# Kernel optimization log

Measured on AMD Instinct MI355X. Metric: run time of the kernel, lower is better.

## Reference

```python
import jax, jax.numpy as jnp
import numpy as np

# Shapes / hyperparams (match init_kwargs and input_specs)
B, CIN, COUT, H, W = 8, 128, 128, 64, 64
K, S, P, D = 3, 1, 1, 1
KK = K * K
EPS = 1e-5  # BatchNorm eps


def setup_inputs() -> dict:
    key = jax.random.key(0)
    ks = jax.random.split(key, 4)
    x = jax.random.normal(ks[0], (B, CIN, H, W), jnp.float32)
    # small offset weights so predicted offsets stay O(1) pixels
    w_off = jax.random.normal(ks[1], (2 * KK, CIN, K, K), jnp.float32) * 0.01
    w_def = jax.random.normal(ks[2], (COUT, CIN, K, K), jnp.float32) * (1.0 / np.sqrt(CIN * KK))
    b_def = jax.random.normal(ks[3], (COUT,), jnp.float32) * 0.01
    gamma = jnp.ones((COUT,), jnp.float32)
    beta = jnp.zeros((COUT,), jnp.float32)
    return dict(x=x, w_off=w_off, w_def=w_def, b_def=b_def, gamma=gamma, beta=beta)


def _bilinear_gather(x, ys, xs):
    """x: [B,C,H,W]; ys/xs: [B,KK,Ho,Wo] float coords -> [B,C,KK,Ho,Wo].
    Zero padding outside the image (torchvision DeformConv2d semantics)."""
    Bb, C, Hh, Ww = x.shape
    y0 = jnp.floor(ys)
    x0 = jnp.floor(xs)
    wy = ys - y0
    wx = xs - x0
    xf = x.reshape(Bb, C, Hh * Ww)

    def gather(yi, xi, w):
        valid = (yi >= 0) & (yi < Hh) & (xi >= 0) & (xi < Ww)
        idx = (jnp.clip(yi, 0, Hh - 1) * Ww + jnp.clip(xi, 0, Ww - 1)).astype(jnp.int32)
        g = jnp.take_along_axis(xf, idx.reshape(Bb, 1, -1), axis=2)  # [B,C,KK*Ho*Wo]
        g = g.reshape(Bb, C, *idx.shape[1:])  # [B,C,KK,Ho,Wo]
        return g * (w * valid)[:, None]

    return (gather(y0, x0, (1 - wy) * (1 - wx))
            + gather(y0, x0 + 1, (1 - wy) * wx)
            + gather(y0 + 1, x0, wy * (1 - wx))
            + gather(y0 + 1, x0 + 1, wy * wx))


def _forward(x, w_off, w_def, b_def, gamma, beta):
    # 1) offset prediction: standard conv, no bias
    offset = jax.lax.conv_general_dilated(
        x, w_off, window_strides=(S, S), padding=((P, P), (P, P)),
        rhs_dilation=(D, D), dimension_numbers=('NCHW', 'OIHW', 'NCHW'))
    Ho, Wo = offset.shape[2], offset.shape[3]
    off = offset.reshape(B, KK, 2, Ho, Wo)  # (dy, dx) pairs per kernel loc
    dy, dx = off[:, :, 0], off[:, :, 1]

    # 2) deformable sampling coordinates
    ky = (jnp.arange(KK) // K).astype(jnp.float32) * D  # kernel row offset
    kx = (jnp.arange(KK) % K).astype(jnp.float32) * D   # kernel col offset
    base_y = (jnp.arange(Ho) * S - P).astype(jnp.float32)
    base_x = (jnp.arange(Wo) * S - P).astype(jnp.float32)
    ys = base_y[None, None, :, None] + ky[None, :, None, None] + dy  # [B,KK,Ho,Wo]
    xs = base_x[None, None, None, :] + kx[None, :, None, None] + dx

    sampled = _bilinear_gather(x, ys, xs)  # [B,CIN,KK,Ho,Wo]

    # 3) per-kernel-location weighted accumulation (implicit GEMM) + bias
    out = jnp.einsum('bckhw,ock->bohw', sampled, w_def.reshape(COUT, CIN, KK))
    out = out + b_def[None, :, None, None]

    # 4) BatchNorm2d (training mode: batch statistics) + SiLU
    mean = out.mean(axis=(0, 2, 3))
    var = out.var(axis=(0, 2, 3))
    scale = gamma / jnp.sqrt(var + EPS)
    out = (out - mean[None, :, None, None]) * scale[None, :, None, None] + beta[None, :, None, None]
    return out * jax.nn.sigmoid(out)  # SiLU


def reference(x, w_off, w_def, b_def, gamma, beta):
    return _forward(x, w_off, w_def, b_def, gamma, beta)
```

## Files before the change

kernel.cpp:

```cpp
#include <hip/hip_runtime.h>
#include <math.h>

#define CIN   128
#define COUT  128
#define KKT   9
#define NSTAT 32768.0f

typedef __attribute__((ext_vector_type(8))) short bf16x8;
typedef __attribute__((ext_vector_type(4))) float f32x4;

__device__ inline unsigned short f2bf(float f) {
    union { float f; unsigned u; } v; v.f = f;
    unsigned r = v.u + 0x7fffu + ((v.u >> 16) & 1u);
    return (unsigned short)(r >> 16);
}
__device__ inline float bflo(unsigned u) { union { unsigned u; float f; } v; v.u = u << 16; return v.f; }
__device__ inline float bfhi(unsigned u) { union { unsigned u; float f; } v; v.u = u & 0xffff0000u; return v.f; }

#define FAST_BARRIER() asm volatile("s_waitcnt lgkmcnt(0)\n\ts_barrier" ::: "memory")


__global__ __launch_bounds__(512) void prep_xt_k(const float* __restrict__ x,
                                                 unsigned* __restrict__ xt) {
    __shared__ float lt[128][65];
    const int by = blockIdx.x;
    const int b = by >> 6, y = by & 63;
    const int t = threadIdx.x, l = t & 63, g8 = t >> 6;
    const float* xb = x + (b * 128) * 4096 + y * 64;
#pragma unroll
    for (int pass = 0; pass < 16; pass++) {
        int c = pass * 8 + g8;
        lt[c][l] = xb[c * 4096 + l];
    }
    __syncthreads();
    unsigned* xo = xt + (by * 64) * 64;
#pragma unroll
    for (int pass = 0; pass < 8; pass++) {
        int w = pass * 8 + g8;
        float f0 = lt[2 * l][w], f1 = lt[2 * l + 1][w];
        xo[w * 64 + l] = (unsigned)f2bf(f0) | ((unsigned)f2bf(f1) << 16);
    }
}

__global__ __launch_bounds__(256) void repack_w_k(const float* __restrict__ w_def,
                                                  const float* __restrict__ w_off,
                                                  unsigned short* __restrict__ wb,
                                                  unsigned short* __restrict__ wob,
                                                  float* __restrict__ sums) {
    int i = blockIdx.x * 256 + threadIdx.x;
    if (i < 147456) {
        int oc = i / 1152, r = i - oc * 1152, kt = r >> 7, c = r & 127;
        wb[i] = f2bf(w_def[(oc * 128 + c) * 9 + kt]);
    } else if (i < 147456 + 36864) {
        int j = i - 147456;
        int ocp = j / 1152, r = j - ocp * 1152, kt = r >> 7, c = r & 127;
        wob[j] = (ocp < 18) ? f2bf(w_off[(ocp * 128 + c) * 9 + kt]) : (unsigned short)0;
    } else if (i < 147456 + 36864 + 256) {
        sums[i - 147456 - 36864] = 0.f;
    }
}

#define RB 51200
__global__ __launch_bounds__(512, 4) void deform_main_k(const unsigned* __restrict__ xt,
                                                        const unsigned short* __restrict__ wb,
                                                        const unsigned short* __restrict__ wob,
                                                        const float* __restrict__ b_def,
                                                        float* __restrict__ out,
                                                        float* __restrict__ sums,
                                                        float* __restrict__ sumsq) {
    __shared__ __align__(16) unsigned char smem[RB + 4608 + 1024];
    unsigned short* xrow = (unsigned short*)smem;
    int*            tab  = (int*)smem;
    unsigned short* samp0 = (unsigned short*)(smem + 18432);
    unsigned short* samp1 = (unsigned short*)(smem + 34816);
    float* offl = (float*)(smem + RB);
    float* stat = (float*)(smem + RB + 4608);

    const int t    = threadIdx.x;
    const int bh   = blockIdx.x;
    const int b    = bh >> 6;
    const int j_   = bh & 63;
    const int h    = ((j_ & 7) << 3) | (j_ >> 3);
    const int lane = t & 63;
    const int wv   = __builtin_amdgcn_readfirstlane(t >> 6);
    const int quad = lane >> 4, lo = lane & 15;
    const int l    = lane;
    const int g    = lane >> 2;

    if (t < 256) stat[t] = 0.f;

    const unsigned* xtb = xt + b * 262144;

    for (int p = wv; p < 198; p += 8) {
        int r = p / 66, xi = p - r * 66;
        int y = h + r - 1, x = xi - 1;
        unsigned u = 0;
        if ((unsigned)y < 64u && (unsigned)x < 64u) u = xtb[(y * 64 + x) * 64 + l];
        ((unsigned*)xrow)[(r * 66 + xi) * 64 + ((g ^ (xi & 15)) << 2) + (l & 3)] = u;
    }
    __syncthreads();

    {
        const int mt = wv >> 2, nt = wv & 3;
        f32x4 ao = {0.f, 0.f, 0.f, 0.f};
        const unsigned short* wrow = wob + (mt * 16 + lo) * 1152 + quad * 8;
        for (int kt = 0; kt < 9; kt++) {
            int ky = kt / 3, kx = kt - ky * 3;
            int xi = nt * 16 + lo + kx;
#pragma unroll
            for (int ch = 0; ch < 4; ch++) {
                int gg = ch * 4 + quad;
                bf16x8 af = *(const bf16x8*)(wrow + kt * 128 + ch * 32);
                bf16x8 bf = *(const bf16x8*)(xrow + (ky * 66 + xi) * 128 + ((gg ^ (xi & 15)) << 3));
                ao = __builtin_amdgcn_mfma_f32_16x16x32_bf16(af, bf, ao, 0, 0, 0);
            }
        }
        __syncthreads();
#pragma unroll
        for (int r = 0; r < 4; r++) {
            int oc = mt * 16 + quad * 4 + r;
            if (oc < 18) offl[oc * 64 + nt * 16 + lo] = ao[r];
        }
    }
    __syncthreads();

    for (int i = t; i < KKT * 64; i += 512) {
        int k = i >> 6, w2 = i & 63;
        float dy = offl[(2 * k) * 64 + w2];
        float dx = offl[(2 * k + 1) * 64 + w2];
        int ky = k / 3, kx = k - ky * 3;
        float ys = (float)(h - 1 + ky) + dy;
        float xs = (float)(w2 - 1 + kx) + dx;
        float y0f = floorf(ys), x0f = floorf(xs);
        float wyf = ys - y0f, wxf = xs - x0f;
        int iy0 = (int)y0f, ix0 = (int)x0f;
        int cy0 = min(max(iy0, 0), 63), cy1 = min(max(iy0 + 1, 0), 63);
        int px  = min(max(ix0, 0), 63), px2 = min(max(ix0 + 1, 0), 63);
        float wy0 = (iy0 >= 0 && iy0 < 64) ? (1.f - wyf) : 0.f;
        float wy1 = (iy0 + 1 >= 0 && iy0 + 1 < 64) ? wyf : 0.f;
        float wa  = (ix0 >= 0 && ix0 < 64) ? (1.f - wxf) : 0.f;
        float wbv = (ix0 + 1 >= 0 && ix0 + 1 < 64) ? wxf : 0.f;
        int base = i * 8;
        tab[base + 0] = (cy0 * 64 + px ) * 64;
        tab[base + 1] = (cy0 * 64 + px2) * 64;
        tab[base + 2] = (cy1 * 64 + px ) * 64;
        tab[base + 3] = (cy1 * 64 + px2) * 64;
        ((float*)tab)[base + 4] = wy0;
        ((float*)tab)[base + 5] = wy1;
        ((float*)tab)[base + 6] = wa;
        ((float*)tab)[base + 7] = wbv;
    }
    __syncthreads();

    const int m0 = wv >> 1, n0 = wv & 1;
    f32x4 acc[2][2];
#pragma unroll
    for (int i = 0; i < 2; i++)
#pragma unroll
        for (int j = 0; j < 2; j++)
#pragma unroll
            for (int r = 0; r < 4; r++) acc[i][j][r] = 0.f;

    const unsigned short* wrow0 = wb + (2 * m0 * 16 + lo) * 1152 + quad * 8;
    const unsigned short* wrow1 = wrow0 + 16 * 1152;

    for (int kt = 0; kt < KKT; kt++) {
        bf16x8 af0[4], af1[4];
#pragma unroll
        for (int ch = 0; ch < 4; ch++) {
            af0[ch] = *(const bf16x8*)(wrow0 + kt * 128 + ch * 32);
            af1[ch] = *(const bf16x8*)(wrow1 + kt * 128 + ch * 32);
        }
        unsigned* sb = (unsigned*)((kt & 1) ? samp1 : samp0);
#pragma unroll
        for (int i = 0; i < 8; i++) {
            int w = wv * 8 + i;
            int bse = (kt * 64 + w) * 8;
            int4   ta = *(const int4*)&tab[bse];
            float4 tw = *(const float4*)&tab[bse + 4];
            unsigned u00 = xtb[ta.x + l];
            unsigned u01 = xtb[ta.y + l];
            unsigned u10 = xtb[ta.z + l];
            unsigned u11 = xtb[ta.w + l];
            float e = tw.x * (tw.z * bflo(u00) + tw.w * bflo(u01)) +
                      tw.y * (tw.z * bflo(u10) + tw.w * bflo(u11));
            float o = tw.x * (tw.z * bfhi(u00) + tw.w * bfhi(u01)) +
                      tw.y * (tw.z * bfhi(u10) + tw.w * bfhi(u11));
            sb[w * 64 + ((g ^ (w & 15)) << 2) + (l & 3)] =
                (unsigned)f2bf(e) | ((unsigned)f2bf(o) << 16);
        }
        FAST_BARRIER();
        const unsigned short* sbs = (kt & 1) ? samp1 : samp0;
#pragma unroll
        for (int ch = 0; ch < 4; ch++) {
            int gg = ch * 4 + quad;
            int r0 = (2 * n0 + 0) * 16 + lo, r1 = (2 * n0 + 1) * 16 + lo;
            bf16x8 bf0 = *(const bf16x8*)(sbs + r0 * 128 + ((gg ^ lo) << 3));
            bf16x8 bf1 = *(const bf16x8*)(sbs + r1 * 128 + ((gg ^ lo) << 3));
            acc[0][0] = __builtin_amdgcn_mfma_f32_16x16x32_bf16(af0[ch], bf0, acc[0][0], 0, 0, 0);
            acc[0][1] = __builtin_amdgcn_mfma_f32_16x16x32_bf16(af0[ch], bf1, acc[0][1], 0, 0, 0);
            acc[1][0] = __builtin_amdgcn_mfma_f32_16x16x32_bf16(af1[ch], bf0, acc[1][0], 0, 0, 0);
            acc[1][1] = __builtin_amdgcn_mfma_f32_16x16x32_bf16(af1[ch], bf1, acc[1][1], 0, 0, 0);
        }
    }

    float* ob = out + b * COUT * 4096 + h * 64;
#pragma unroll
    for (int mt2 = 0; mt2 < 2; mt2++) {
        int ocb = (2 * m0 + mt2) * 16 + quad * 4;
#pragma unroll
        for (int r = 0; r < 4; r++) {
            int oc = ocb + r;
            float bia = b_def[oc];
            float ssum = 0.f, qsum = 0.f;
#pragma unroll
            for (int nt2 = 0; nt2 < 2; nt2++) {
                int w_ = (2 * n0 + nt2) * 16 + lo;
                float v = acc[mt2][nt2][r] + bia;
                ob[oc * 4096 + w_] = v;
                ssum += v; qsum += v * v;
            }
#pragma unroll
            for (int d = 1; d < 16; d <<= 1) {
                ssum += __shfl_xor(ssum, d, 64);
                qsum += __shfl_xor(qsum, d, 64);
            }
            if (lo == 0) { atomicAdd(&stat[oc], ssum); atomicAdd(&stat[128 + oc], qsum); }
        }
    }
    __syncthreads();
    if (t < 256) {
        float* gp = (t < 128) ? (sums + t) : (sumsq + (t - 128));
        atomicAdd(gp, stat[t]);
    }
}

__global__ __launch_bounds__(256) void bn_silu_k(float* __restrict__ out,
                                                 const float* __restrict__ sums,
                                                 const float* __restrict__ sumsq,
                                                 const float* __restrict__ gamma,
                                                 const float* __restrict__ beta) {
    __shared__ float sc_s[128], sh_s[128];
    int t = threadIdx.x;
    if (t < 128) {
        const float invN = 1.f / NSTAT;
        float m = sums[t] * invN;
        float v = fmaf(-m, m, sumsq[t] * invN);
        float sc = gamma[t] * rsqrtf(v + 1e-5f);
        sc_s[t] = sc;
        sh_s[t] = beta[t] - m * sc;
    }
    __syncthreads();
    int i = blockIdx.x * 256 + t;
    float4 v = ((float4*)out)[i];
    int oc = (i >> 10) & 127;
    float sc = sc_s[oc], sh = sh_s[oc];
    float z0 = v.x * sc + sh;
    float z1 = v.y * sc + sh;
    float z2 = v.z * sc + sh;
    float z3 = v.w * sc + sh;
    v.x = z0 / (1.f + __expf(-z0));
    v.y = z1 / (1.f + __expf(-z1));
    v.z = z2 / (1.f + __expf(-z2));
    v.w = z3 / (1.f + __expf(-z3));
    ((float4*)out)[i] = v;
}

extern "C" void kernel_launch(void* const* d_in, const int* in_sizes, int n_in,
                              void* d_out, int out_size, void* d_ws, size_t ws_size,
                              hipStream_t stream) {
    const float* x     = (const float*)d_in[0];
    const float* w_off = (const float*)d_in[1];
    const float* w_def = (const float*)d_in[2];
    const float* b_def = (const float*)d_in[3];
    const float* gamma = (const float*)d_in[4];
    const float* beta  = (const float*)d_in[5];
    float* out = (float*)d_out;

    unsigned*       xt   = (unsigned*)d_ws;
    unsigned short* wb   = (unsigned short*)((char*)d_ws + 16777216);
    unsigned short* wob  = (unsigned short*)((char*)d_ws + 17072128);
    float*          sums = (float*)((char*)d_ws + 17145856);
    float*          sumsq = sums + 128;

    prep_xt_k<<<512, 512, 0, stream>>>(x, xt);
    repack_w_k<<<721, 256, 0, stream>>>(w_def, w_off, wb, wob, sums);
    deform_main_k<<<512, 512, 0, stream>>>(xt, wb, wob, b_def, out, sums, sumsq);
    bn_silu_k<<<4096, 256, 0, stream>>>(out, sums, sumsq, gamma, beta);
}
```

Measured before the change: 167.9 us.

## Merge prep kernels and software-pipeline gather and weight loads across kernel taps

The input transpose and the weight repack kernels become a single launch, removing one kernel launch and its gap. In the main deformable conv loop, the four bilinear-corner gathers and the weight fragments for the next tap are issued before the barrier and MFMA phase of the current tap, so their memory latency overlaps with compute. This holds 32 extra gathered words plus the weight fragments in registers, which may reduce occupancy under the 512x4 launch bound or cause spills.

```diff
diff --git a/kernel.cpp b/kernel.cpp
--- a/kernel.cpp
+++ b/kernel.cpp
@@ -20,43 +20,45 @@
 #define FAST_BARRIER() asm volatile("s_waitcnt lgkmcnt(0)\n\ts_barrier" ::: "memory")
 
 
-__global__ __launch_bounds__(512) void prep_xt_k(const float* __restrict__ x,
-                                                 unsigned* __restrict__ xt) {
-    __shared__ float lt[128][65];
-    const int by = blockIdx.x;
-    const int b = by >> 6, y = by & 63;
-    const int t = threadIdx.x, l = t & 63, g8 = t >> 6;
-    const float* xb = x + (b * 128) * 4096 + y * 64;
-#pragma unroll
-    for (int pass = 0; pass < 16; pass++) {
-        int c = pass * 8 + g8;
-        lt[c][l] = xb[c * 4096 + l];
-    }
-    __syncthreads();
-    unsigned* xo = xt + (by * 64) * 64;
-#pragma unroll
-    for (int pass = 0; pass < 8; pass++) {
-        int w = pass * 8 + g8;
-        float f0 = lt[2 * l][w], f1 = lt[2 * l + 1][w];
-        xo[w * 64 + l] = (unsigned)f2bf(f0) | ((unsigned)f2bf(f1) << 16);
-    }
-}
-
-__global__ __launch_bounds__(256) void repack_w_k(const float* __restrict__ w_def,
+__global__ __launch_bounds__(512) void prep_all_k(const float* __restrict__ x,
+                                                  const float* __restrict__ w_def,
                                                   const float* __restrict__ w_off,
+                                                  unsigned* __restrict__ xt,
                                                   unsigned short* __restrict__ wb,
                                                   unsigned short* __restrict__ wob,
                                                   float* __restrict__ sums) {
-    int i = blockIdx.x * 256 + threadIdx.x;
-    if (i < 147456) {
-        int oc = i / 1152, r = i - oc * 1152, kt = r >> 7, c = r & 127;
-        wb[i] = f2bf(w_def[(oc * 128 + c) * 9 + kt]);
-    } else if (i < 147456 + 36864) {
-        int j = i - 147456;
-        int ocp = j / 1152, r = j - ocp * 1152, kt = r >> 7, c = r & 127;
-        wob[j] = (ocp < 18) ? f2bf(w_off[(ocp * 128 + c) * 9 + kt]) : (unsigned short)0;
-    } else if (i < 147456 + 36864 + 256) {
-        sums[i - 147456 - 36864] = 0.f;
+    const int blk = blockIdx.x;
+    if (blk < 512) {
+        __shared__ float lt[128][65];
+        const int by = blk;
+        const int b = by >> 6, y = by & 63;
+        const int t = threadIdx.x, l = t & 63, g8 = t >> 6;
+        const float* xb = x + (b * 128) * 4096 + y * 64;
+#pragma unroll
+        for (int pass = 0; pass < 16; pass++) {
+            int c = pass * 8 + g8;
+            lt[c][l] = xb[c * 4096 + l];
+        }
+        __syncthreads();
+        unsigned* xo = xt + (by * 64) * 64;
+#pragma unroll
+        for (int pass = 0; pass < 8; pass++) {
+            int w = pass * 8 + g8;
+            float f0 = lt[2 * l][w], f1 = lt[2 * l + 1][w];
+            xo[w * 64 + l] = (unsigned)f2bf(f0) | ((unsigned)f2bf(f1) << 16);
+        }
+    } else {
+        int i = (blk - 512) * 512 + threadIdx.x;
+        if (i < 147456) {
+            int oc = i / 1152, r = i - oc * 1152, kt = r >> 7, c = r & 127;
+            wb[i] = f2bf(w_def[(oc * 128 + c) * 9 + kt]);
+        } else if (i < 147456 + 36864) {
+            int j = i - 147456;
+            int ocp = j / 1152, r = j - ocp * 1152, kt = r >> 7, c = r & 127;
+            wob[j] = (ocp < 18) ? f2bf(w_off[(ocp * 128 + c) * 9 + kt]) : (unsigned short)0;
+        } else if (i < 147456 + 36864 + 256) {
+            sums[i - 147456 - 36864] = 0.f;
+        }
     }
 }
 
@@ -164,24 +166,32 @@
     const unsigned short* wrow0 = wb + (2 * m0 * 16 + lo) * 1152 + quad * 8;
     const unsigned short* wrow1 = wrow0 + 16 * 1152;
 
+    unsigned gr[32];
+    bf16x8 afA[4], afB[4];
+
+#pragma unroll
+    for (int i = 0; i < 8; i++) {
+        int w = wv * 8 + i;
+        int4 ta = *(const int4*)&tab[(0 * 64 + w) * 8];
+        gr[i * 4 + 0] = xtb[ta.x + l];
+        gr[i * 4 + 1] = xtb[ta.y + l];
+        gr[i * 4 + 2] = xtb[ta.z + l];
+        gr[i * 4 + 3] = xtb[ta.w + l];
+    }
+#pragma unroll
+    for (int ch = 0; ch < 4; ch++) {
+        afA[ch] = *(const bf16x8*)(wrow0 + 0 * 128 + ch * 32);
+        afB[ch] = *(const bf16x8*)(wrow1 + 0 * 128 + ch * 32);
+    }
+
     for (int kt = 0; kt < KKT; kt++) {
-        bf16x8 af0[4], af1[4];
-#pragma unroll
-        for (int ch = 0; ch < 4; ch++) {
-            af0[ch] = *(const bf16x8*)(wrow0 + kt * 128 + ch * 32);
-            af1[ch] = *(const bf16x8*)(wrow1 + kt * 128 + ch * 32);
-        }
         unsigned* sb = (unsigned*)((kt & 1) ? samp1 : samp0);
 #pragma unroll
         for (int i = 0; i < 8; i++) {
             int w = wv * 8 + i;
-            int bse = (kt * 64 + w) * 8;
-            int4   ta = *(const int4*)&tab[bse];
-            float4 tw = *(const float4*)&tab[bse + 4];
-            unsigned u00 = xtb[ta.x + l];
-            unsigned u01 = xtb[ta.y + l];
-            unsigned u10 = xtb[ta.z + l];
-            unsigned u11 = xtb[ta.w + l];
+            float4 tw = *(const float4*)&tab[(kt * 64 + w) * 8 + 4];
+            unsigned u00 = gr[i * 4 + 0], u01 = gr[i * 4 + 1];
+            unsigned u10 = gr[i * 4 + 2], u11 = gr[i * 4 + 3];
             float e = tw.x * (tw.z * bflo(u00) + tw.w * bflo(u01)) +
                       tw.y * (tw.z * bflo(u10) + tw.w * bflo(u11));
             float o = tw.x * (tw.z * bfhi(u00) + tw.w * bfhi(u01)) +
@@ -189,6 +199,17 @@
             sb[w * 64 + ((g ^ (w & 15)) << 2) + (l & 3)] =
                 (unsigned)f2bf(e) | ((unsigned)f2bf(o) << 16);
         }
+        if (kt < KKT - 1) {
+#pragma unroll
+            for (int i = 0; i < 8; i++) {
+                int w = wv * 8 + i;
+                int4 ta = *(const int4*)&tab[((kt + 1) * 64 + w) * 8];
+                gr[i * 4 + 0] = xtb[ta.x + l];
+                gr[i * 4 + 1] = xtb[ta.y + l];
+                gr[i * 4 + 2] = xtb[ta.z + l];
+                gr[i * 4 + 3] = xtb[ta.w + l];
+            }
+        }
         FAST_BARRIER();
         const unsigned short* sbs = (kt & 1) ? samp1 : samp0;
 #pragma unroll
@@ -197,10 +218,17 @@
             int r0 = (2 * n0 + 0) * 16 + lo, r1 = (2 * n0 + 1) * 16 + lo;
             bf16x8 bf0 = *(const bf16x8*)(sbs + r0 * 128 + ((gg ^ lo) << 3));
             bf16x8 bf1 = *(const bf16x8*)(sbs + r1 * 128 + ((gg ^ lo) << 3));
-            acc[0][0] = __builtin_amdgcn_mfma_f32_16x16x32_bf16(af0[ch], bf0, acc[0][0], 0, 0, 0);
-            acc[0][1] = __builtin_amdgcn_mfma_f32_16x16x32_bf16(af0[ch], bf1, acc[0][1], 0, 0, 0);
-            acc[1][0] = __builtin_amdgcn_mfma_f32_16x16x32_bf16(af1[ch], bf0, acc[1][0], 0, 0, 0);
-            acc[1][1] = __builtin_amdgcn_mfma_f32_16x16x32_bf16(af1[ch], bf1, acc[1][1], 0, 0, 0);
+            acc[0][0] = __builtin_amdgcn_mfma_f32_16x16x32_bf16(afA[ch], bf0, acc[0][0], 0, 0, 0);
+            acc[0][1] = __builtin_amdgcn_mfma_f32_16x16x32_bf16(afA[ch], bf1, acc[0][1], 0, 0, 0);
+            acc[1][0] = __builtin_amdgcn_mfma_f32_16x16x32_bf16(afB[ch], bf0, acc[1][0], 0, 0, 0);
+            acc[1][1] = __builtin_amdgcn_mfma_f32_16x16x32_bf16(afB[ch], bf1, acc[1][1], 0, 0, 0);
+        }
+        if (kt < KKT - 1) {
+#pragma unroll
+            for (int ch = 0; ch < 4; ch++) {
+                afA[ch] = *(const bf16x8*)(wrow0 + (kt + 1) * 128 + ch * 32);
+                afB[ch] = *(const bf16x8*)(wrow1 + (kt + 1) * 128 + ch * 32);
+            }
         }
     }
 
@@ -283,8 +311,7 @@
     float*          sums = (float*)((char*)d_ws + 17145856);
     float*          sumsq = sums + 128;
 
-    prep_xt_k<<<512, 512, 0, stream>>>(x, xt);
-    repack_w_k<<<721, 256, 0, stream>>>(w_def, w_off, wb, wob, sums);
+    prep_all_k<<<873, 512, 0, stream>>>(x, w_def, w_off, xt, wb, wob, sums);
     deform_main_k<<<512, 512, 0, stream>>>(xt, wb, wob, b_def, out, sums, sumsq);
     bn_silu_k<<<4096, 256, 0, stream>>>(out, sums, sumsq, gamma, beta);
 }
```

After: 181.7 us. +8.2%, slower.

## Gather deformable samples directly into MFMA registers, drop LDS staging and merge prep kernels

Applied to the files above, without the earlier changes.

The main kernel now uses 256 threads. Each wave owns 16 output columns and all 128 output channels. The offset conv and the bilinear sampling read x straight from global memory into MFMA B-fragments in registers, instead of staging the input rows and sampled tiles in LDS behind per-tap barriers. The two prep kernels are merged into one launch, and bf16 packing uses a cheaper rounding. In exchange there are more redundant global/L2 loads, many more weight fragment loads per wave, more register pressure from 8 accumulators, and slightly different bf16 rounding.

```diff
diff --git a/kernel.cpp b/kernel.cpp
--- a/kernel.cpp
+++ b/kernel.cpp
@@ -9,6 +9,8 @@
 typedef __attribute__((ext_vector_type(8))) short bf16x8;
 typedef __attribute__((ext_vector_type(4))) float f32x4;
 
+union U4B { uint4 u; bf16x8 b; };
+
 __device__ inline unsigned short f2bf(float f) {
     union { float f; unsigned u; } v; v.f = f;
     unsigned r = v.u + 0x7fffu + ((v.u >> 16) & 1u);
@@ -16,65 +18,65 @@
 }
 __device__ inline float bflo(unsigned u) { union { unsigned u; float f; } v; v.u = u << 16; return v.f; }
 __device__ inline float bfhi(unsigned u) { union { unsigned u; float f; } v; v.u = u & 0xffff0000u; return v.f; }
-
-#define FAST_BARRIER() asm volatile("s_waitcnt lgkmcnt(0)\n\ts_barrier" ::: "memory")
-
-
-__global__ __launch_bounds__(512) void prep_xt_k(const float* __restrict__ x,
-                                                 unsigned* __restrict__ xt) {
-    __shared__ float lt[128][65];
-    const int by = blockIdx.x;
-    const int b = by >> 6, y = by & 63;
-    const int t = threadIdx.x, l = t & 63, g8 = t >> 6;
-    const float* xb = x + (b * 128) * 4096 + y * 64;
-#pragma unroll
-    for (int pass = 0; pass < 16; pass++) {
-        int c = pass * 8 + g8;
-        lt[c][l] = xb[c * 4096 + l];
-    }
-    __syncthreads();
-    unsigned* xo = xt + (by * 64) * 64;
-#pragma unroll
-    for (int pass = 0; pass < 8; pass++) {
-        int w = pass * 8 + g8;
-        float f0 = lt[2 * l][w], f1 = lt[2 * l + 1][w];
-        xo[w * 64 + l] = (unsigned)f2bf(f0) | ((unsigned)f2bf(f1) << 16);
-    }
-}
-
-__global__ __launch_bounds__(256) void repack_w_k(const float* __restrict__ w_def,
+__device__ inline unsigned pk2bf(float e, float o) {
+    union { float f; unsigned u; } a, b; a.f = e; b.f = o;
+    return ((a.u + 0x8000u) >> 16) | ((b.u + 0x8000u) & 0xffff0000u);
+}
+
+
+__global__ __launch_bounds__(512) void prep_all_k(const float* __restrict__ x,
+                                                  const float* __restrict__ w_def,
                                                   const float* __restrict__ w_off,
+                                                  unsigned* __restrict__ xt,
                                                   unsigned short* __restrict__ wb,
                                                   unsigned short* __restrict__ wob,
                                                   float* __restrict__ sums) {
-    int i = blockIdx.x * 256 + threadIdx.x;
-    if (i < 147456) {
-        int oc = i / 1152, r = i - oc * 1152, kt = r >> 7, c = r & 127;
-        wb[i] = f2bf(w_def[(oc * 128 + c) * 9 + kt]);
-    } else if (i < 147456 + 36864) {
-        int j = i - 147456;
-        int ocp = j / 1152, r = j - ocp * 1152, kt = r >> 7, c = r & 127;
-        wob[j] = (ocp < 18) ? f2bf(w_off[(ocp * 128 + c) * 9 + kt]) : (unsigned short)0;
-    } else if (i < 147456 + 36864 + 256) {
-        sums[i - 147456 - 36864] = 0.f;
-    }
-}
-
-#define RB 51200
-__global__ __launch_bounds__(512, 4) void deform_main_k(const unsigned* __restrict__ xt,
+    const int blk = blockIdx.x;
+    if (blk < 512) {
+        __shared__ float lt[128][65];
+        const int by = blk;
+        const int b = by >> 6, y = by & 63;
+        const int t = threadIdx.x, l = t & 63, g8 = t >> 6;
+        const float* xb = x + (b * 128) * 4096 + y * 64;
+#pragma unroll
+        for (int pass = 0; pass < 16; pass++) {
+            int c = pass * 8 + g8;
+            lt[c][l] = xb[c * 4096 + l];
+        }
+        __syncthreads();
+        unsigned* xo = xt + (by * 64) * 64;
+#pragma unroll
+        for (int pass = 0; pass < 8; pass++) {
+            int w = pass * 8 + g8;
+            float f0 = lt[2 * l][w], f1 = lt[2 * l + 1][w];
+            xo[w * 64 + l] = (unsigned)f2bf(f0) | ((unsigned)f2bf(f1) << 16);
+        }
+    } else {
+        int i = (blk - 512) * 512 + threadIdx.x;
+        if (i < 147456) {
+            int oc = i / 1152, r = i - oc * 1152, kt = r >> 7, c = r & 127;
+            wb[i] = f2bf(w_def[(oc * 128 + c) * 9 + kt]);
+        } else if (i < 147456 + 36864) {
+            int j = i - 147456;
+            int ocp = j / 1152, r = j - ocp * 1152, kt = r >> 7, c = r & 127;
+            wob[j] = (ocp < 18) ? f2bf(w_off[(ocp * 128 + c) * 9 + kt]) : (unsigned short)0;
+        } else if (i < 147456 + 36864 + 256) {
+            sums[i - 147456 - 36864] = 0.f;
+        }
+    }
+}
+
+__global__ __launch_bounds__(256, 2) void deform_main_k(const unsigned* __restrict__ xt,
                                                         const unsigned short* __restrict__ wb,
                                                         const unsigned short* __restrict__ wob,
                                                         const float* __restrict__ b_def,
                                                         float* __restrict__ out,
                                                         float* __restrict__ sums,
                                                         float* __restrict__ sumsq) {
-    __shared__ __align__(16) unsigned char smem[RB + 4608 + 1024];
-    unsigned short* xrow = (unsigned short*)smem;
-    int*            tab  = (int*)smem;
-    unsigned short* samp0 = (unsigned short*)(smem + 18432);
-    unsigned short* samp1 = (unsigned short*)(smem + 34816);
-    float* offl = (float*)(smem + RB);
-    float* stat = (float*)(smem + RB + 4608);
+    __shared__ int   taddr[KKT][64][4];
+    __shared__ float twts[KKT][64][4];
+    __shared__ float offl[18][64];
+    __shared__ float stat[256];
 
     const int t    = threadIdx.x;
     const int bh   = blockIdx.x;
@@ -84,50 +86,47 @@
     const int lane = t & 63;
     const int wv   = __builtin_amdgcn_readfirstlane(t >> 6);
     const int quad = lane >> 4, lo = lane & 15;
-    const int l    = lane;
-    const int g    = lane >> 2;
-
-    if (t < 256) stat[t] = 0.f;
+    const int w    = wv * 16 + lo;
+
+    stat[t] = 0.f;
 
     const unsigned* xtb = xt + b * 262144;
 
-    for (int p = wv; p < 198; p += 8) {
-        int r = p / 66, xi = p - r * 66;
-        int y = h + r - 1, x = xi - 1;
-        unsigned u = 0;
-        if ((unsigned)y < 64u && (unsigned)x < 64u) u = xtb[(y * 64 + x) * 64 + l];
-        ((unsigned*)xrow)[(r * 66 + xi) * 64 + ((g ^ (xi & 15)) << 2) + (l & 3)] = u;
-    }
-    __syncthreads();
-
     {
-        const int mt = wv >> 2, nt = wv & 3;
-        f32x4 ao = {0.f, 0.f, 0.f, 0.f};
-        const unsigned short* wrow = wob + (mt * 16 + lo) * 1152 + quad * 8;
+        f32x4 a0 = {0.f, 0.f, 0.f, 0.f}, a1 = {0.f, 0.f, 0.f, 0.f};
+        const unsigned short* wr0 = wob + lo * 1152 + quad * 8;
+        const unsigned short* wr1 = wob + (16 + lo) * 1152 + quad * 8;
         for (int kt = 0; kt < 9; kt++) {
             int ky = kt / 3, kx = kt - ky * 3;
-            int xi = nt * 16 + lo + kx;
+            int y  = h + ky - 1;
+            int xp = w + kx - 1;
+            bool val = ((unsigned)y < 64u) && ((unsigned)xp < 64u);
+            int py = min(max(y, 0), 63), px = min(max(xp, 0), 63);
+            const unsigned* pb = xtb + (py * 64 + px) * 64;
 #pragma unroll
             for (int ch = 0; ch < 4; ch++) {
-                int gg = ch * 4 + quad;
-                bf16x8 af = *(const bf16x8*)(wrow + kt * 128 + ch * 32);
-                bf16x8 bf = *(const bf16x8*)(xrow + (ky * 66 + xi) * 128 + ((gg ^ (xi & 15)) << 3));
-                ao = __builtin_amdgcn_mfma_f32_16x16x32_bf16(af, bf, ao, 0, 0, 0);
-            }
-        }
-        __syncthreads();
+                U4B bu; bu.u = *(const uint4*)(pb + ch * 16 + quad * 4);
+                if (!val) { bu.u.x = 0; bu.u.y = 0; bu.u.z = 0; bu.u.w = 0; }
+                bf16x8 af0 = *(const bf16x8*)(wr0 + kt * 128 + ch * 32);
+                bf16x8 af1 = *(const bf16x8*)(wr1 + kt * 128 + ch * 32);
+                a0 = __builtin_amdgcn_mfma_f32_16x16x32_bf16(af0, bu.b, a0, 0, 0, 0);
+                a1 = __builtin_amdgcn_mfma_f32_16x16x32_bf16(af1, bu.b, a1, 0, 0, 0);
+            }
+        }
 #pragma unroll
         for (int r = 0; r < 4; r++) {
-            int oc = mt * 16 + quad * 4 + r;
-            if (oc < 18) offl[oc * 64 + nt * 16 + lo] = ao[r];
-        }
-    }
-    __syncthreads();
-
-    for (int i = t; i < KKT * 64; i += 512) {
+            int oc0 = quad * 4 + r;
+            if (oc0 < 18) offl[oc0][w] = a0[r];
+            int oc1 = 16 + quad * 4 + r;
+            if (oc1 < 18) offl[oc1][w] = a1[r];
+        }
+    }
+    __syncthreads();
+
+    for (int i = t; i < KKT * 64; i += 256) {
         int k = i >> 6, w2 = i & 63;
-        float dy = offl[(2 * k) * 64 + w2];
-        float dx = offl[(2 * k + 1) * 64 + w2];
+        float dy = offl[2 * k][w2];
+        float dx = offl[2 * k + 1][w2];
         int ky = k / 3, kx = k - ky * 3;
         float ys = (float)(h - 1 + ky) + dy;
         float xs = (float)(w2 - 1 + kx) + dx;
@@ -140,96 +139,89 @@
         float wy1 = (iy0 + 1 >= 0 && iy0 + 1 < 64) ? wyf : 0.f;
         float wa  = (ix0 >= 0 && ix0 < 64) ? (1.f - wxf) : 0.f;
         float wbv = (ix0 + 1 >= 0 && ix0 + 1 < 64) ? wxf : 0.f;
-        int base = i * 8;
-        tab[base + 0] = (cy0 * 64 + px ) * 64;
-        tab[base + 1] = (cy0 * 64 + px2) * 64;
-        tab[base + 2] = (cy1 * 64 + px ) * 64;
-        tab[base + 3] = (cy1 * 64 + px2) * 64;
-        ((float*)tab)[base + 4] = wy0;
-        ((float*)tab)[base + 5] = wy1;
-        ((float*)tab)[base + 6] = wa;
-        ((float*)tab)[base + 7] = wbv;
-    }
-    __syncthreads();
-
-    const int m0 = wv >> 1, n0 = wv & 1;
-    f32x4 acc[2][2];
-#pragma unroll
-    for (int i = 0; i < 2; i++)
-#pragma unroll
-        for (int j = 0; j < 2; j++)
-#pragma unroll
-            for (int r = 0; r < 4; r++) acc[i][j][r] = 0.f;
-
-    const unsigned short* wrow0 = wb + (2 * m0 * 16 + lo) * 1152 + quad * 8;
-    const unsigned short* wrow1 = wrow0 + 16 * 1152;
+        taddr[k][w2][0] = (cy0 * 64 + px ) * 64;
+        taddr[k][w2][1] = (cy0 * 64 + px2) * 64;
+        taddr[k][w2][2] = (cy1 * 64 + px ) * 64;
+        taddr[k][w2][3] = (cy1 * 64 + px2) * 64;
+        twts[k][w2][0] = wy0;
+        twts[k][w2][1] = wy1;
+        twts[k][w2][2] = wa;
+        twts[k][w2][3] = wbv;
+    }
+    __syncthreads();
+
+    f32x4 acc[8];
+#pragma unroll
+    for (int i = 0; i < 8; i++) acc[i] = (f32x4){0.f, 0.f, 0.f, 0.f};
+
+    const unsigned short* wlq = wb + lo * 1152 + quad * 8;
 
     for (int kt = 0; kt < KKT; kt++) {
-        bf16x8 af0[4], af1[4];
+        int4   ta = *(const int4*)&taddr[kt][w][0];
+        float4 tw = *(const float4*)&twts[kt][w][0];
+        float c00 = tw.x * tw.z, c01 = tw.x * tw.w;
+        float c10 = tw.y * tw.z, c11 = tw.y * tw.w;
+        const unsigned* p00 = xtb + ta.x;
+        const unsigned* p01 = xtb + ta.y;
+        const unsigned* p10 = xtb + ta.z;
+        const unsigned* p11 = xtb + ta.w;
+        const unsigned short* wk = wlq + kt * 128;
 #pragma unroll
         for (int ch = 0; ch < 4; ch++) {
-            af0[ch] = *(const bf16x8*)(wrow0 + kt * 128 + ch * 32);
-            af1[ch] = *(const bf16x8*)(wrow1 + kt * 128 + ch * 32);
-        }
-        unsigned* sb = (unsigned*)((kt & 1) ? samp1 : samp0);
-#pragma unroll
-        for (int i = 0; i < 8; i++) {
-            int w = wv * 8 + i;
-            int bse = (kt * 64 + w) * 8;
-            int4   ta = *(const int4*)&tab[bse];
-            float4 tw = *(const float4*)&tab[bse + 4];
-            unsigned u00 = xtb[ta.x + l];
-            unsigned u01 = xtb[ta.y + l];
-            unsigned u10 = xtb[ta.z + l];
-            unsigned u11 = xtb[ta.w + l];
-            float e = tw.x * (tw.z * bflo(u00) + tw.w * bflo(u01)) +
-                      tw.y * (tw.z * bflo(u10) + tw.w * bflo(u11));
-            float o = tw.x * (tw.z * bfhi(u00) + tw.w * bfhi(u01)) +
-                      tw.y * (tw.z * bfhi(u10) + tw.w * bfhi(u11));
-            sb[w * 64 + ((g ^ (w & 15)) << 2) + (l & 3)] =
-                (unsigned)f2bf(e) | ((unsigned)f2bf(o) << 16);
-        }
-        FAST_BARRIER();
-        const unsigned short* sbs = (kt & 1) ? samp1 : samp0;
-#pragma unroll
-        for (int ch = 0; ch < 4; ch++) {
-            int gg = ch * 4 + quad;
-            int r0 = (2 * n0 + 0) * 16 + lo, r1 = (2 * n0 + 1) * 16 + lo;
-            bf16x8 bf0 = *(const bf16x8*)(sbs + r0 * 128 + ((gg ^ lo) << 3));
-            bf16x8 bf1 = *(const bf16x8*)(sbs + r1 * 128 + ((gg ^ lo) << 3));
-            acc[0][0] = __builtin_amdgcn_mfma_f32_16x16x32_bf16(af0[ch], bf0, acc[0][0], 0, 0, 0);
-            acc[0][1] = __builtin_amdgcn_mfma_f32_16x16x32_bf16(af0[ch], bf1, acc[0][1], 0, 0, 0);
-            acc[1][0] = __builtin_amdgcn_mfma_f32_16x16x32_bf16(af1[ch], bf0, acc[1][0], 0, 0, 0);
-            acc[1][1] = __builtin_amdgcn_mfma_f32_16x16x32_bf16(af1[ch], bf1, acc[1][1], 0, 0, 0);
+            int off = ch * 16 + quad * 4;
+            uint4 u00 = *(const uint4*)(p00 + off);
+            uint4 u01 = *(const uint4*)(p01 + off);
+            uint4 u10 = *(const uint4*)(p10 + off);
+            uint4 u11 = *(const uint4*)(p11 + off);
+            U4B bf;
+            {
+                float e = c00 * bflo(u00.x) + c01 * bflo(u01.x) + c10 * bflo(u10.x) + c11 * bflo(u11.x);
+                float o = c00 * bfhi(u00.x) + c01 * bfhi(u01.x) + c10 * bfhi(u10.x) + c11 * bfhi(u11.x);
+                bf.u.x = pk2bf(e, o);
+            }
+            {
+                float e = c00 * bflo(u00.y) + c01 * bflo(u01.y) + c10 * bflo(u10.y) + c11 * bflo(u11.y);
+                float o = c00 * bfhi(u00.y) + c01 * bfhi(u01.y) + c10 * bfhi(u10.y) + c11 * bfhi(u11.y);
+                bf.u.y = pk2bf(e, o);
+            }
+            {
+                float e = c00 * bflo(u00.z) + c01 * bflo(u01.z) + c10 * bflo(u10.z) + c11 * bflo(u11.z);
+                float o = c00 * bfhi(u00.z) + c01 * bfhi(u01.z) + c10 * bfhi(u10.z) + c11 * bfhi(u11.z);
+                bf.u.z = pk2bf(e, o);
+            }
+            {
+                float e = c00 * bflo(u00.w) + c01 * bflo(u01.w) + c10 * bflo(u10.w) + c11 * bflo(u11.w);
+                float o = c00 * bfhi(u00.w) + c01 * bfhi(u01.w) + c10 * bfhi(u10.w) + c11 * bfhi(u11.w);
+                bf.u.w = pk2bf(e, o);
+            }
+            const unsigned short* wkc = wk + ch * 32;
+#pragma unroll
+            for (int mt = 0; mt < 8; mt++) {
+                bf16x8 af = *(const bf16x8*)(wkc + mt * 16 * 1152);
+                acc[mt] = __builtin_amdgcn_mfma_f32_16x16x32_bf16(af, bf.b, acc[mt], 0, 0, 0);
+            }
         }
     }
 
     float* ob = out + b * COUT * 4096 + h * 64;
 #pragma unroll
-    for (int mt2 = 0; mt2 < 2; mt2++) {
-        int ocb = (2 * m0 + mt2) * 16 + quad * 4;
+    for (int mt = 0; mt < 8; mt++) {
 #pragma unroll
         for (int r = 0; r < 4; r++) {
-            int oc = ocb + r;
-            float bia = b_def[oc];
-            float ssum = 0.f, qsum = 0.f;
-#pragma unroll
-            for (int nt2 = 0; nt2 < 2; nt2++) {
-                int w_ = (2 * n0 + nt2) * 16 + lo;
-                float v = acc[mt2][nt2][r] + bia;
-                ob[oc * 4096 + w_] = v;
-                ssum += v; qsum += v * v;
-            }
+            int oc = mt * 16 + quad * 4 + r;
+            float v = acc[mt][r] + b_def[oc];
+            ob[oc * 4096 + w] = v;
+            float s = v, q = v * v;
 #pragma unroll
             for (int d = 1; d < 16; d <<= 1) {
-                ssum += __shfl_xor(ssum, d, 64);
-                qsum += __shfl_xor(qsum, d, 64);
-            }
-            if (lo == 0) { atomicAdd(&stat[oc], ssum); atomicAdd(&stat[128 + oc], qsum); }
-        }
-    }
-    __syncthreads();
-    if (t < 256) {
+                s += __shfl_xor(s, d, 64);
+                q += __shfl_xor(q, d, 64);
+            }
+            if (lo == 0) { atomicAdd(&stat[oc], s); atomicAdd(&stat[128 + oc], q); }
+        }
+    }
+    __syncthreads();
+    {
         float* gp = (t < 128) ? (sums + t) : (sumsq + (t - 128));
         atomicAdd(gp, stat[t]);
     }
@@ -283,8 +275,7 @@
     float*          sums = (float*)((char*)d_ws + 17145856);
     float*          sumsq = sums + 128;
 
-    prep_xt_k<<<512, 512, 0, stream>>>(x, xt);
-    repack_w_k<<<721, 256, 0, stream>>>(w_def, w_off, wb, wob, sums);
-    deform_main_k<<<512, 512, 0, stream>>>(xt, wb, wob, b_def, out, sums, sumsq);
+    prep_all_k<<<873, 512, 0, stream>>>(x, w_def, w_off, xt, wb, wob, sums);
+    deform_main_k<<<512, 256, 0, stream>>>(xt, wb, wob, b_def, out, sums, sumsq);
     bn_silu_k<<<4096, 256, 0, stream>>>(out, sums, sumsq, gamma, beta);
 }
```

Result: slower. 219.1 us (+30.4%).

## Merge prep kernels and drop halo staging to shrink LDS in deform kernel

Applied to the files above, without the earlier changes.

Fuses the x transpose and weight repack kernels into one launch, saving a kernel launch. In the main kernel the offset-prediction conv now reads its B operand straight from global memory instead of staging a 3-row halo in LDS. That shrinks shared memory from about 57KB to roughly 52KB and raises the launch-bounds occupancy hint from 4 to 6. The tradeoff is uncoalesced-ish global loads in the offset conv in exchange for possibly more resident blocks per CU.

```diff
diff --git a/kernel.cpp b/kernel.cpp
--- a/kernel.cpp
+++ b/kernel.cpp
@@ -9,6 +9,8 @@
 typedef __attribute__((ext_vector_type(8))) short bf16x8;
 typedef __attribute__((ext_vector_type(4))) float f32x4;
 
+union U4B { uint4 u; bf16x8 b; };
+
 __device__ inline unsigned short f2bf(float f) {
     union { float f; unsigned u; } v; v.f = f;
     unsigned r = v.u + 0x7fffu + ((v.u >> 16) & 1u);
@@ -20,61 +22,60 @@
 #define FAST_BARRIER() asm volatile("s_waitcnt lgkmcnt(0)\n\ts_barrier" ::: "memory")
 
 
-__global__ __launch_bounds__(512) void prep_xt_k(const float* __restrict__ x,
-                                                 unsigned* __restrict__ xt) {
-    __shared__ float lt[128][65];
-    const int by = blockIdx.x;
-    const int b = by >> 6, y = by & 63;
-    const int t = threadIdx.x, l = t & 63, g8 = t >> 6;
-    const float* xb = x + (b * 128) * 4096 + y * 64;
-#pragma unroll
-    for (int pass = 0; pass < 16; pass++) {
-        int c = pass * 8 + g8;
-        lt[c][l] = xb[c * 4096 + l];
-    }
-    __syncthreads();
-    unsigned* xo = xt + (by * 64) * 64;
-#pragma unroll
-    for (int pass = 0; pass < 8; pass++) {
-        int w = pass * 8 + g8;
-        float f0 = lt[2 * l][w], f1 = lt[2 * l + 1][w];
-        xo[w * 64 + l] = (unsigned)f2bf(f0) | ((unsigned)f2bf(f1) << 16);
-    }
-}
-
-__global__ __launch_bounds__(256) void repack_w_k(const float* __restrict__ w_def,
+__global__ __launch_bounds__(512) void prep_all_k(const float* __restrict__ x,
+                                                  const float* __restrict__ w_def,
                                                   const float* __restrict__ w_off,
+                                                  unsigned* __restrict__ xt,
                                                   unsigned short* __restrict__ wb,
                                                   unsigned short* __restrict__ wob,
                                                   float* __restrict__ sums) {
-    int i = blockIdx.x * 256 + threadIdx.x;
-    if (i < 147456) {
-        int oc = i / 1152, r = i - oc * 1152, kt = r >> 7, c = r & 127;
-        wb[i] = f2bf(w_def[(oc * 128 + c) * 9 + kt]);
-    } else if (i < 147456 + 36864) {
-        int j = i - 147456;
-        int ocp = j / 1152, r = j - ocp * 1152, kt = r >> 7, c = r & 127;
-        wob[j] = (ocp < 18) ? f2bf(w_off[(ocp * 128 + c) * 9 + kt]) : (unsigned short)0;
-    } else if (i < 147456 + 36864 + 256) {
-        sums[i - 147456 - 36864] = 0.f;
-    }
-}
-
-#define RB 51200
-__global__ __launch_bounds__(512, 4) void deform_main_k(const unsigned* __restrict__ xt,
+    const int blk = blockIdx.x;
+    if (blk < 512) {
+        __shared__ float lt[128][65];
+        const int by = blk;
+        const int b = by >> 6, y = by & 63;
+        const int t = threadIdx.x, l = t & 63, g8 = t >> 6;
+        const float* xb = x + (b * 128) * 4096 + y * 64;
+#pragma unroll
+        for (int pass = 0; pass < 16; pass++) {
+            int c = pass * 8 + g8;
+            lt[c][l] = xb[c * 4096 + l];
+        }
+        __syncthreads();
+        unsigned* xo = xt + (by * 64) * 64;
+#pragma unroll
+        for (int pass = 0; pass < 8; pass++) {
+            int w = pass * 8 + g8;
+            float f0 = lt[2 * l][w], f1 = lt[2 * l + 1][w];
+            xo[w * 64 + l] = (unsigned)f2bf(f0) | ((unsigned)f2bf(f1) << 16);
+        }
+    } else {
+        int i = (blk - 512) * 512 + threadIdx.x;
+        if (i < 147456) {
+            int oc = i / 1152, r = i - oc * 1152, kt = r >> 7, c = r & 127;
+            wb[i] = f2bf(w_def[(oc * 128 + c) * 9 + kt]);
+        } else if (i < 147456 + 36864) {
+            int j = i - 147456;
+            int ocp = j / 1152, r = j - ocp * 1152, kt = r >> 7, c = r & 127;
+            wob[j] = (ocp < 18) ? f2bf(w_off[(ocp * 128 + c) * 9 + kt]) : (unsigned short)0;
+        } else if (i < 147456 + 36864 + 256) {
+            sums[i - 147456 - 36864] = 0.f;
+        }
+    }
+}
+
+__global__ __launch_bounds__(512, 6) void deform_main_k(const unsigned* __restrict__ xt,
                                                         const unsigned short* __restrict__ wb,
                                                         const unsigned short* __restrict__ wob,
                                                         const float* __restrict__ b_def,
                                                         float* __restrict__ out,
                                                         float* __restrict__ sums,
                                                         float* __restrict__ sumsq) {
-    __shared__ __align__(16) unsigned char smem[RB + 4608 + 1024];
-    unsigned short* xrow = (unsigned short*)smem;
-    int*            tab  = (int*)smem;
-    unsigned short* samp0 = (unsigned short*)(smem + 18432);
-    unsigned short* samp1 = (unsigned short*)(smem + 34816);
-    float* offl = (float*)(smem + RB);
-    float* stat = (float*)(smem + RB + 4608);
+    __shared__ int   taddr[KKT][64][4];
+    __shared__ float twts[KKT][64][4];
+    __shared__ __align__(16) unsigned short samp[2][64][128];
+    __shared__ float stat[256];
+    float* offl = (float*)&samp[0][0][0];
 
     const int t    = threadIdx.x;
     const int bh   = blockIdx.x;
@@ -91,35 +92,31 @@
 
     const unsigned* xtb = xt + b * 262144;
 
-    for (int p = wv; p < 198; p += 8) {
-        int r = p / 66, xi = p - r * 66;
-        int y = h + r - 1, x = xi - 1;
-        unsigned u = 0;
-        if ((unsigned)y < 64u && (unsigned)x < 64u) u = xtb[(y * 64 + x) * 64 + l];
-        ((unsigned*)xrow)[(r * 66 + xi) * 64 + ((g ^ (xi & 15)) << 2) + (l & 3)] = u;
-    }
-    __syncthreads();
-
     {
-        const int mt = wv >> 2, nt = wv & 3;
+        const int nt = wv & 3, mt = wv >> 2;
+        const int wpix = nt * 16 + lo;
         f32x4 ao = {0.f, 0.f, 0.f, 0.f};
-        const unsigned short* wrow = wob + (mt * 16 + lo) * 1152 + quad * 8;
+        const unsigned short* wr = wob + (mt * 16 + lo) * 1152 + quad * 8;
         for (int kt = 0; kt < 9; kt++) {
             int ky = kt / 3, kx = kt - ky * 3;
-            int xi = nt * 16 + lo + kx;
+            int y  = h + ky - 1;
+            int xp = wpix + kx - 1;
+            bool val = ((unsigned)y < 64u) && ((unsigned)xp < 64u);
+            int py = min(max(y, 0), 63), px = min(max(xp, 0), 63);
+            const unsigned* pb = xtb + (py * 64 + px) * 64;
 #pragma unroll
             for (int ch = 0; ch < 4; ch++) {
-                int gg = ch * 4 + quad;
-                bf16x8 af = *(const bf16x8*)(wrow + kt * 128 + ch * 32);
-                bf16x8 bf = *(const bf16x8*)(xrow + (ky * 66 + xi) * 128 + ((gg ^ (xi & 15)) << 3));
-                ao = __builtin_amdgcn_mfma_f32_16x16x32_bf16(af, bf, ao, 0, 0, 0);
+                U4B bu; bu.u = *(const uint4*)(pb + ch * 16 + quad * 4);
+                if (!val) { bu.u.x = 0; bu.u.y = 0; bu.u.z = 0; bu.u.w = 0; }
+                bf16x8 af = *(const bf16x8*)(wr + kt * 128 + ch * 32);
+                ao = __builtin_amdgcn_mfma_f32_16x16x32_bf16(af, bu.b, ao, 0, 0, 0);
             }
         }
         __syncthreads();
 #pragma unroll
         for (int r = 0; r < 4; r++) {
             int oc = mt * 16 + quad * 4 + r;
-            if (oc < 18) offl[oc * 64 + nt * 16 + lo] = ao[r];
+            if (oc < 18) offl[oc * 64 + wpix] = ao[r];
         }
     }
     __syncthreads();
@@ -140,15 +137,14 @@
         float wy1 = (iy0 + 1 >= 0 && iy0 + 1 < 64) ? wyf : 0.f;
         float wa  = (ix0 >= 0 && ix0 < 64) ? (1.f - wxf) : 0.f;
         float wbv = (ix0 + 1 >= 0 && ix0 + 1 < 64) ? wxf : 0.f;
-        int base = i * 8;
-        tab[base + 0] = (cy0 * 64 + px ) * 64;
-        tab[base + 1] = (cy0 * 64 + px2) * 64;
-        tab[base + 2] = (cy1 * 64 + px ) * 64;
-        tab[base + 3] = (cy1 * 64 + px2) * 64;
-        ((float*)tab)[base + 4] = wy0;
-        ((float*)tab)[base + 5] = wy1;
-        ((float*)tab)[base + 6] = wa;
-        ((float*)tab)[base + 7] = wbv;
+        taddr[k][w2][0] = (cy0 * 64 + px ) * 64;
+        taddr[k][w2][1] = (cy0 * 64 + px2) * 64;
+        taddr[k][w2][2] = (cy1 * 64 + px ) * 64;
+        taddr[k][w2][3] = (cy1 * 64 + px2) * 64;
+        twts[k][w2][0] = wy0;
+        twts[k][w2][1] = wy1;
+        twts[k][w2][2] = wa;
+        twts[k][w2][3] = wbv;
     }
     __syncthreads();
 
@@ -171,13 +167,12 @@
             af0[ch] = *(const bf16x8*)(wrow0 + kt * 128 + ch * 32);
             af1[ch] = *(const bf16x8*)(wrow1 + kt * 128 + ch * 32);
         }
-        unsigned* sb = (unsigned*)((kt & 1) ? samp1 : samp0);
+        unsigned* sb = (unsigned*)&samp[kt & 1][0][0];
 #pragma unroll
         for (int i = 0; i < 8; i++) {
             int w = wv * 8 + i;
-            int bse = (kt * 64 + w) * 8;
-            int4   ta = *(const int4*)&tab[bse];
-            float4 tw = *(const float4*)&tab[bse + 4];
+            int4   ta = *(const int4*)&taddr[kt][w][0];
+            float4 tw = *(const float4*)&twts[kt][w][0];
             unsigned u00 = xtb[ta.x + l];
             unsigned u01 = xtb[ta.y + l];
             unsigned u10 = xtb[ta.z + l];
@@ -190,7 +185,7 @@
                 (unsigned)f2bf(e) | ((unsigned)f2bf(o) << 16);
         }
         FAST_BARRIER();
-        const unsigned short* sbs = (kt & 1) ? samp1 : samp0;
+        const unsigned short* sbs = &samp[kt & 1][0][0];
 #pragma unroll
         for (int ch = 0; ch < 4; ch++) {
             int gg = ch * 4 + quad;
@@ -283,8 +278,7 @@
     float*          sums = (float*)((char*)d_ws + 17145856);
     float*          sumsq = sums + 128;
 
-    prep_xt_k<<<512, 512, 0, stream>>>(x, xt);
-    repack_w_k<<<721, 256, 0, stream>>>(w_def, w_off, wb, wob, sums);
+    prep_all_k<<<873, 512, 0, stream>>>(x, w_def, w_off, xt, wb, wob, sums);
     deform_main_k<<<512, 512, 0, stream>>>(xt, wb, wob, b_def, out, sums, sumsq);
     bn_silu_k<<<4096, 256, 0, stream>>>(out, sums, sumsq, gamma, beta);
 }
```

Measured after the change: 173.6 us. 1.03x slower.
